# Performance work log

Measured on AMD Instinct MI355X. Metric: run time of the kernel, lower is better.

Reference implementation:

```python
import jax, jax.numpy as jnp
import numpy as np

B, P, K = 32, 2048, 20   # events, points per event, kNN neighbors
EPS = 1e-5               # BatchNorm eps (eval mode, running stats)


def setup_inputs() -> dict:
    key = jax.random.key(0)
    ks = iter(jax.random.split(key, 64))
    inp = {}
    inp["x"] = jax.random.normal(next(ks), (B * P, 7), jnp.float32)
    inp["batch"] = jnp.repeat(jnp.arange(B, dtype=jnp.int32), P)

    def add_layer(tag, cin, cout):
        inp["w" + tag] = jax.random.normal(next(ks), (cin, cout), jnp.float32) / np.sqrt(cin)
        inp["b" + tag] = jax.random.normal(next(ks), (cout,), jnp.float32) * 0.01
        inp["g" + tag] = jax.random.uniform(next(ks), (cout,), jnp.float32, 0.5, 1.5)
        inp["e" + tag] = jax.random.normal(next(ks), (cout,), jnp.float32) * 0.1
        inp["m" + tag] = jax.random.normal(next(ks), (cout,), jnp.float32) * 0.1
        inp["v" + tag] = jax.random.uniform(next(ks), (cout,), jnp.float32, 0.5, 1.5)

    # conv1 MLP: [14, 64, 64, 64]
    add_layer("10", 14, 64)
    add_layer("11", 64, 64)
    add_layer("12", 64, 64)
    # conv2 MLP: [128, 128]
    add_layer("20", 128, 128)
    return inp


def _lin_relu_bn(h, W, b, g, be, rm, rv):
    # Linear -> ReLU -> BatchNorm1d (eval mode: running stats)
    h = jax.nn.relu(h @ W + b)
    return (h - rm) * (g / jnp.sqrt(rv + EPS)) + be


def _knn_idx(x):
    # x: [B, P, C] -> indices of K nearest neighbors (incl. self), [B, P, K]
    sq = jnp.sum(x * x, axis=-1)                                   # [B, P]
    d = sq[:, :, None] + sq[:, None, :] - 2.0 * jnp.einsum("bpc,bqc->bpq", x, x)
    _, idx = jax.lax.top_k(-d, K)
    return idx


def _edge_conv(x, mlp):
    # DynamicEdgeConv: kNN graph on current features, edge MLP([x_i, x_j - x_i]), max-aggr
    idx = _knn_idx(x)                                              # [B, P, K]
    xj = jax.vmap(lambda xb, ib: xb[ib])(x, idx)                   # [B, P, K, C]
    xi = jnp.broadcast_to(x[:, :, None, :], xj.shape)
    e = jnp.concatenate([xi, xj - xi], axis=-1)                    # [B, P, K, 2C]
    return jnp.max(mlp(e), axis=2)                                 # [B, P, Cout]


def reference(x, batch,
              w10, b10, g10, e10, m10, v10,
              w11, b11, g11, e11, m11, v11,
              w12, b12, g12, e12, m12, v12,
              w20, b20, g20, e20, m20, v20):
    xb = x.reshape(B, P, -1)                                       # fixed-size events

    def mlp1(e):
        h = _lin_relu_bn(e, w10, b10, g10, e10, m10, v10)
        h = _lin_relu_bn(h, w11, b11, g11, e11, m11, v11)
        return _lin_relu_bn(h, w12, b12, g12, e12, m12, v12)

    def mlp2(e):
        return _lin_relu_bn(e, w20, b20, g20, e20, m20, v20)

    x1 = _edge_conv(xb, mlp1)                                      # [B, P, 64]
    x2 = _edge_conv(x1, mlp2)                                      # [B, P, 128]
    out = jnp.concatenate([x1, x2], axis=-1).reshape(B * P, 192)
    return out, batch
```

## Files before the change

kernel.cpp:

```cpp
#include <hip/hip_runtime.h>

#define B_EV 32
#define P_PT 2048
#define K_NN 20
#define NPTS (B_EV*P_PT)
#define EPS_BN 1e-5f
#define RINF 3.0e38f

typedef _Float16 half8 __attribute__((ext_vector_type(8)));
typedef float f32x4 __attribute__((ext_vector_type(4)));

static constexpr int oWA10=0, oWB10=448, oB10=896, oT10=960,
  oT11=5184,
  oT12=9408,
  oWA20=9472, oWB20=17664, oB20=25856, oT20=25984,
  oB11p=26048, oB12p=26112,
  oW11hi=26176, oW11lo=28224,
  oW12hi=30272, oW12lo=32320;
static constexpr size_t oIDX = 36864;
static constexpr size_t oA1  = 1347584;
static constexpr size_t oB1  = oA1 + (size_t)NPTS*64;
static constexpr size_t oV2  = oB1 + (size_t)NPTS*64;
static constexpr size_t oX1  = oV2 + (size_t)NPTS*128;
static constexpr size_t oSQ  = oX1 + (size_t)NPTS*64;
static constexpr size_t oX1H = oSQ + (size_t)NPTS;
static constexpr size_t oX1L = oX1H + (size_t)NPTS*32;
static constexpr size_t oU2  = oA1;

__global__ __launch_bounds__(128) void k_prep(
  const float* w10,const float* b10,const float* g10,const float* e10,const float* m10,const float* v10,
  const float* w11,const float* b11,const float* g11,const float* e11,const float* m11,const float* v11,
  const float* w12,const float* b12,const float* g12,const float* e12,const float* m12,const float* v12,
  const float* w20,const float* b20,const float* g20,const float* e20,const float* m20,const float* v20,
  float* ws)
{
  __shared__ float t10s[64], t11s[64];
  int c = threadIdx.x;
  if (c < 64) {
    float s0 = g10[c]*rsqrtf(v10[c]+EPS_BN);
    ws[oB10+c]=b10[c]*s0;
    float t10 = e10[c]-m10[c]*s0; ws[oT10+c]=t10; t10s[c]=t10;
    for (int i=0;i<7;i++){
      ws[oWA10+i*64+c]=(w10[i*64+c]-w10[(7+i)*64+c])*s0;
      ws[oWB10+i*64+c]=w10[(7+i)*64+c]*s0;
    }
    float s1 = g11[c]*rsqrtf(v11[c]+EPS_BN);
    float t11 = e11[c]-m11[c]*s1; ws[oT11+c]=t11; t11s[c]=t11;
    float s2 = g12[c]*rsqrtf(v12[c]+EPS_BN);
    ws[oT12+c]=e12[c]-m12[c]*s2;
  }
  __syncthreads();
  if (c < 64) {
    float s1 = g11[c]*rsqrtf(v11[c]+EPS_BN);
    _Float16* W1hi = (_Float16*)(ws + oW11hi);
    _Float16* W1lo = (_Float16*)(ws + oW11lo);
    float acc = b11[c]*s1;
    for (int i=0;i<64;i++){
      float wv = w11[i*64+c]*s1;
      _Float16 h = (_Float16)wv;
      W1hi[c*64+i] = h;
      W1lo[c*64+i] = (_Float16)(wv - (float)h);
      acc = fmaf(t10s[i], wv, acc);
    }
    ws[oB11p+c]=acc;
    float s2 = g12[c]*rsqrtf(v12[c]+EPS_BN);
    _Float16* W2hi = (_Float16*)(ws + oW12hi);
    _Float16* W2lo = (_Float16*)(ws + oW12lo);
    float acc2 = b12[c]*s2;
    for (int i=0;i<64;i++){
      float wv = w12[i*64+c]*s2;
      _Float16 h = (_Float16)wv;
      W2hi[c*64+i] = h;
      W2lo[c*64+i] = (_Float16)(wv - (float)h);
      acc2 = fmaf(t11s[i], wv, acc2);
    }
    ws[oB12p+c]=acc2;
  }
  {
    float s = g20[c]*rsqrtf(v20[c]+EPS_BN);
    ws[oB20+c]=b20[c]*s; ws[oT20+c]=e20[c]-m20[c]*s;
    for (int i=0;i<64;i++){
      ws[oWA20+i*128+c]=(w20[i*128+c]-w20[(64+i)*128+c])*s;
      ws[oWB20+i*128+c]=w20[(64+i)*128+c]*s;
    }
  }
}

__device__ __forceinline__ void select20(float (&d)[32], int lane, int base, int g,
                                         int* __restrict__ idxout)
{
  float g4[4];
  #pragma unroll
  for (int k=0;k<4;k++){
    float m = d[8*k];
    #pragma unroll
    for (int j=1;j<8;j++) m = fminf(m, d[8*k+j]);
    g4[k]=m;
  }
  float T = 0.f;
  #pragma unroll 1
  for (int pass=0; pass<20; ++pass){
    float m = fminf(fminf(g4[0],g4[1]), fminf(g4[2],g4[3]));
    #pragma unroll
    for (int off=32; off>0; off>>=1) m = fminf(m, __shfl_xor(m, off, 64));
    if (pass==19){ T=m; break; }
    #pragma unroll
    for (int k=0;k<4;k++){
      if (g4[k]==m){
        #pragma unroll
        for (int j=0;j<8;j++) d[8*k+j] = (d[8*k+j]==m) ? RINF : d[8*k+j];
        float mm = d[8*k];
        #pragma unroll
        for (int j=1;j<8;j++) mm = fminf(mm, d[8*k+j]);
        g4[k]=mm;
      }
    }
  }
  int cnt=0;
  #pragma unroll
  for (int j=0;j<32;j++){
    bool take = (d[j]>=RINF) || (d[j]==T);
    unsigned long long mb = __ballot(take);
    if (take){
      int pos = cnt + (int)__popcll(mb & ((1ull<<lane)-1ull));
      if (pos < K_NN) idxout[(size_t)g*K_NN + pos] = base + j*64 + lane;
    }
    cnt += (int)__popcll(mb);
  }
  if (lane==0){
    for (int r=cnt; r<K_NN; ++r) idxout[(size_t)g*K_NN + r] = g;
  }
}

__global__ __launch_bounds__(1024, 8) void k_knn1(const float* __restrict__ x, int* __restrict__ idxout)
{
  __shared__ float xs[P_PT*8];
  int t = threadIdx.x;
  int b = blockIdx.x;
  int xcd = b & 7, kk = b >> 3;
  int e = xcd + ((kk >> 7) << 3);
  int blk = kk & 127;
  {
    const float* xe = x + (size_t)e*P_PT*7;
    #pragma unroll
    for (int u=0; u<2; u++){
      int p = t + u*1024;
      float v0=xe[p*7+0], v1=xe[p*7+1], v2=xe[p*7+2], v3=xe[p*7+3];
      float v4=xe[p*7+4], v5=xe[p*7+5], v6=xe[p*7+6];
      int s = (p&7)<<2;
      int w0 = (p*8) ^ s;
      int w1 = (p*8+4) ^ s;
      f32x4 lo = {v0,v1,v2,v3};
      f32x4 hi = {v4,v5,v6,0.f};
      *(f32x4*)(xs + w0) = lo;
      *(f32x4*)(xs + w1) = hi;
    }
  }
  __syncthreads();
  int lane = t & 63;
  int g = e*P_PT + blk*16 + (t>>6);
  int pin = g & (P_PT-1);
  float xp[7];
  {
    int s = (pin&7)<<2;
    f32x4 lo = *(const f32x4*)(xs + ((pin*8)^s));
    f32x4 hi = *(const f32x4*)(xs + ((pin*8+4)^s));
    xp[0]=lo[0]; xp[1]=lo[1]; xp[2]=lo[2]; xp[3]=lo[3];
    xp[4]=hi[0]; xp[5]=hi[1]; xp[6]=hi[2];
  }
  int sl = (lane&7)<<2;
  const float* base0 = xs + ((lane*8)^sl);
  const float* base1 = xs + ((lane*8+4)^sl);
  float d[32];
  #pragma unroll
  for (int j=0;j<32;j++){
    f32x4 lo = *(const f32x4*)(base0 + j*512);
    f32x4 hi = *(const f32x4*)(base1 + j*512);
    float s=0.f, df;
    df = xp[0]-lo[0]; s=fmaf(df,df,s);
    df = xp[1]-lo[1]; s=fmaf(df,df,s);
    df = xp[2]-lo[2]; s=fmaf(df,df,s);
    df = xp[3]-lo[3]; s=fmaf(df,df,s);
    df = xp[4]-hi[0]; s=fmaf(df,df,s);
    df = xp[5]-hi[1]; s=fmaf(df,df,s);
    df = xp[6]-hi[2]; s=fmaf(df,df,s);
    d[j]=s;
  }
  select20(d, lane, e*P_PT, g, idxout);
}

__global__ __launch_bounds__(256) void k_ab1(const float* __restrict__ x, const float* __restrict__ W,
                                             float* __restrict__ A1, float* __restrict__ B1)
{
  int g = blockIdx.x*256+threadIdx.x;
  float xi[7];
  #pragma unroll
  for (int i=0;i<7;i++) xi[i]=x[(size_t)g*7+i];
  float a[64], b[64];
  #pragma unroll
  for (int c=0;c<64;c++){ a[c]=W[oB10+c]; b[c]=0.f; }
  #pragma unroll
  for (int i=0;i<7;i++){
    #pragma unroll
    for (int c=0;c<64;c++) a[c]=fmaf(xi[i], W[oWA10+i*64+c], a[c]);
    #pragma unroll
    for (int c=0;c<64;c++) b[c]=fmaf(xi[i], W[oWB10+i*64+c], b[c]);
  }
  #pragma unroll
  for (int c=0;c<64;c+=4){
    float4 oa; oa.x=a[c]; oa.y=a[c+1]; oa.z=a[c+2]; oa.w=a[c+3];
    *(float4*)(A1+(size_t)g*64+c)=oa;
    float4 ob; ob.x=b[c]; ob.y=b[c+1]; ob.z=b[c+2]; ob.w=b[c+3];
    *(float4*)(B1+(size_t)g*64+c)=ob;
  }
}

__global__ __launch_bounds__(256, 2) void k_ec1m(const int* __restrict__ idx, const float* __restrict__ ws,
    const float* __restrict__ A1, const float* __restrict__ B1,
    float* __restrict__ x1, _Float16* __restrict__ x1h, _Float16* __restrict__ x1l,
    float* __restrict__ sqv, float* __restrict__ out)
{
  __shared__ float h2s[4][48*64];
  int t = threadIdx.x, w = t>>6, lane = t&63;
  int b = blockIdx.x;
  int xcd = b & 7, kk = b >> 3;
  int ev = xcd + ((kk >> 8) << 3);
  int iA = ev*P_PT + (kk & 255)*8 + w*2;
  int iB = iA + 1;
  int lg = lane>>4, lr = lane&15;

  int jT0 = idx[(size_t)iA*K_NN + lr];
  int jT1 = idx[(size_t)iB*K_NN + lr];
  int a2 = (lr < 4) ? iA*K_NN + 16 + lr : iB*K_NN + 12 + lr;
  a2 = (lr < 8) ? a2 : 0;
  int jT2 = (lr < 8) ? idx[a2] : iA;

  const float* ApA = A1 + (size_t)iA*64;
  const float* ApB = A1 + (size_t)iB*64;
  float4 avA[2][2], avB[2][2], bv[3][2][2];
  const float* Bp0 = B1 + (size_t)jT0*64;
  const float* Bp1 = B1 + (size_t)jT1*64;
  const float* Bp2 = B1 + (size_t)jT2*64;
  #pragma unroll
  for (int ks=0;ks<2;ks++){
    int c0 = ks*32 + lg*8;
    avA[ks][0] = *(const float4*)(ApA+c0); avA[ks][1] = *(const float4*)(ApA+c0+4);
    avB[ks][0] = *(const float4*)(ApB+c0); avB[ks][1] = *(const float4*)(ApB+c0+4);
    bv[0][ks][0] = *(const float4*)(Bp0+c0); bv[0][ks][1] = *(const float4*)(Bp0+c0+4);
    bv[1][ks][0] = *(const float4*)(Bp1+c0); bv[1][ks][1] = *(const float4*)(Bp1+c0+4);
    bv[2][ks][0] = *(const float4*)(Bp2+c0); bv[2][ks][1] = *(const float4*)(Bp2+c0+4);
  }

  bool useB2 = (lr >= 4) && (lr < 8);
  half8 AH[3][2], AL[3][2];
  #pragma unroll
  for (int tile=0;tile<3;tile++){
    #pragma unroll
    for (int ks=0;ks<2;ks++){
      float4 a0, a1;
      if (tile==0){ a0 = avA[ks][0]; a1 = avA[ks][1]; }
      else if (tile==1){ a0 = avB[ks][0]; a1 = avB[ks][1]; }
      else {
        a0.x = useB2 ? avB[ks][0].x : avA[ks][0].x;  a0.y = useB2 ? avB[ks][0].y : avA[ks][0].y;
        a0.z = useB2 ? avB[ks][0].z : avA[ks][0].z;  a0.w = useB2 ? avB[ks][0].w : avA[ks][0].w;
        a1.x = useB2 ? avB[ks][1].x : avA[ks][1].x;  a1.y = useB2 ? avB[ks][1].y : avA[ks][1].y;
        a1.z = useB2 ? avB[ks][1].z : avA[ks][1].z;  a1.w = useB2 ? avB[ks][1].w : avA[ks][1].w;
      }
      float hv[8];
      hv[0]=fmaxf(a0.x+bv[tile][ks][0].x,0.f); hv[1]=fmaxf(a0.y+bv[tile][ks][0].y,0.f);
      hv[2]=fmaxf(a0.z+bv[tile][ks][0].z,0.f); hv[3]=fmaxf(a0.w+bv[tile][ks][0].w,0.f);
      hv[4]=fmaxf(a1.x+bv[tile][ks][1].x,0.f); hv[5]=fmaxf(a1.y+bv[tile][ks][1].y,0.f);
      hv[6]=fmaxf(a1.z+bv[tile][ks][1].z,0.f); hv[7]=fmaxf(a1.w+bv[tile][ks][1].w,0.f);
      half8 ah, al;
      #pragma unroll
      for (int q=0;q<8;q++){
        _Float16 h = (_Float16)hv[q];
        ah[q]=h; al[q]=(_Float16)(hv[q]-(float)h);
      }
      AH[tile][ks]=ah; AL[tile][ks]=al;
    }
  }

  f32x4 acc[3][4];
  #pragma unroll
  for (int nt=0;nt<4;nt++){
    float bb = ws[oB11p + nt*16 + lr];
    f32x4 v = {bb,bb,bb,bb};
    acc[0][nt]=v; acc[1][nt]=v; acc[2][nt]=v;
  }
  {
    const _Float16* W1hi = (const _Float16*)(ws + oW11hi);
    const _Float16* W1lo = (const _Float16*)(ws + oW11lo);
    #pragma unroll
    for (int nt=0;nt<4;nt++){
      const _Float16* whp = W1hi + (nt*16+lr)*64 + lg*8;
      const _Float16* wlp = W1lo + (nt*16+lr)*64 + lg*8;
      half8 wh0 = *(const half8*)(whp);
      half8 wh1 = *(const half8*)(whp+32);
      half8 wl0 = *(const half8*)(wlp);
      half8 wl1 = *(const half8*)(wlp+32);
      #pragma unroll
      for (int tile=0;tile<3;tile++){
        acc[tile][nt] = __builtin_amdgcn_mfma_f32_16x16x32_f16(AH[tile][0], wh0, acc[tile][nt], 0,0,0);
        acc[tile][nt] = __builtin_amdgcn_mfma_f32_16x16x32_f16(AL[tile][0], wh0, acc[tile][nt], 0,0,0);
        acc[tile][nt] = __builtin_amdgcn_mfma_f32_16x16x32_f16(AH[tile][0], wl0, acc[tile][nt], 0,0,0);
        acc[tile][nt] = __builtin_amdgcn_mfma_f32_16x16x32_f16(AH[tile][1], wh1, acc[tile][nt], 0,0,0);
        acc[tile][nt] = __builtin_amdgcn_mfma_f32_16x16x32_f16(AL[tile][1], wh1, acc[tile][nt], 0,0,0);
        acc[tile][nt] = __builtin_amdgcn_mfma_f32_16x16x32_f16(AH[tile][1], wl1, acc[tile][nt], 0,0,0);
      }
    }
  }

  float* hb = h2s[w];
  #pragma unroll
  for (int tile=0;tile<3;tile++){
    #pragma unroll
    for (int nt=0;nt<4;nt++){
      #pragma unroll
      for (int r=0;r<4;r++){
        int row = tile*16 + lg*4 + r;
        int col = nt*16 + lr;
        int baddr = (row*256 + col*4) ^ ((row&7)<<4);
        *(float*)((char*)hb + baddr) = fmaxf(acc[tile][nt][r], 0.f);
      }
    }
  }

  half8 AH2[3][2], AL2[3][2];
  #pragma unroll
  for (int tile=0;tile<3;tile++){
    #pragma unroll
    for (int ks=0;ks<2;ks++){
      int row = tile*16 + lr;
      int byte0 = (row*256 + (ks*32 + lg*8)*4);
      int s = (row&7)<<4;
      f32x4 v0 = *(const f32x4*)((char*)hb + ((byte0)^s));
      f32x4 v1 = *(const f32x4*)((char*)hb + ((byte0+16)^s));
      half8 ah, al;
      #pragma unroll
      for (int q=0;q<4;q++){
        _Float16 h = (_Float16)v0[q];
        ah[q]=h; al[q]=(_Float16)(v0[q]-(float)h);
      }
      #pragma unroll
      for (int q=0;q<4;q++){
        _Float16 h = (_Float16)v1[q];
        ah[4+q]=h; al[4+q]=(_Float16)(v1[q]-(float)h);
      }
      AH2[tile][ks]=ah; AL2[tile][ks]=al;
    }
  }

  f32x4 acc2[3][4];
  #pragma unroll
  for (int nt=0;nt<4;nt++){
    float bb = ws[oB12p + nt*16 + lr];
    f32x4 v = {bb,bb,bb,bb};
    acc2[0][nt]=v; acc2[1][nt]=v; acc2[2][nt]=v;
  }
  {
    const _Float16* W2hi = (const _Float16*)(ws + oW12hi);
    const _Float16* W2lo = (const _Float16*)(ws + oW12lo);
    #pragma unroll
    for (int nt=0;nt<4;nt++){
      const _Float16* whp = W2hi + (nt*16+lr)*64 + lg*8;
      const _Float16* wlp = W2lo + (nt*16+lr)*64 + lg*8;
      half8 wh0 = *(const half8*)(whp);
      half8 wh1 = *(const half8*)(whp+32);
      half8 wl0 = *(const half8*)(wlp);
      half8 wl1 = *(const half8*)(wlp+32);
      #pragma unroll
      for (int tile=0;tile<3;tile++){
        acc2[tile][nt] = __builtin_amdgcn_mfma_f32_16x16x32_f16(AH2[tile][0], wh0, acc2[tile][nt], 0,0,0);
        acc2[tile][nt] = __builtin_amdgcn_mfma_f32_16x16x32_f16(AL2[tile][0], wh0, acc2[tile][nt], 0,0,0);
        acc2[tile][nt] = __builtin_amdgcn_mfma_f32_16x16x32_f16(AH2[tile][0], wl0, acc2[tile][nt], 0,0,0);
        acc2[tile][nt] = __builtin_amdgcn_mfma_f32_16x16x32_f16(AH2[tile][1], wh1, acc2[tile][nt], 0,0,0);
        acc2[tile][nt] = __builtin_amdgcn_mfma_f32_16x16x32_f16(AL2[tile][1], wh1, acc2[tile][nt], 0,0,0);
        acc2[tile][nt] = __builtin_amdgcn_mfma_f32_16x16x32_f16(AH2[tile][1], wl1, acc2[tile][nt], 0,0,0);
      }
    }
  }

  float finA[4], finB[4];
  float sqA = 0.f, sqB = 0.f;
  #pragma unroll
  for (int nt=0;nt<4;nt++){
    float cvA = -RINF;
    #pragma unroll
    for (int r=0;r<4;r++) cvA = fmaxf(cvA, acc2[0][nt][r]);
    if (lg==0){
      #pragma unroll
      for (int r=0;r<4;r++) cvA = fmaxf(cvA, acc2[2][nt][r]);
    }
    cvA = fmaxf(cvA, __shfl_xor(cvA,16,64));
    cvA = fmaxf(cvA, __shfl_xor(cvA,32,64));
    finA[nt] = fmaxf(cvA, 0.f) + ws[oT12 + nt*16 + lr];
    sqA = fmaf(finA[nt], finA[nt], sqA);

    float cvB = -RINF;
    #pragma unroll
    for (int r=0;r<4;r++) cvB = fmaxf(cvB, acc2[1][nt][r]);
    if (lg==1){
      #pragma unroll
      for (int r=0;r<4;r++) cvB = fmaxf(cvB, acc2[2][nt][r]);
    }
    cvB = fmaxf(cvB, __shfl_xor(cvB,16,64));
    cvB = fmaxf(cvB, __shfl_xor(cvB,32,64));
    finB[nt] = fmaxf(cvB, 0.f) + ws[oT12 + nt*16 + lr];
    sqB = fmaf(finB[nt], finB[nt], sqB);
  }
  if (lane < 16){
    #pragma unroll
    for (int nt=0;nt<4;nt++){
      x1[(size_t)iA*64 + nt*16 + lane] = finA[nt];
      out[(size_t)iA*192 + nt*16 + lane] = finA[nt];
      x1[(size_t)iB*64 + nt*16 + lane] = finB[nt];
      out[(size_t)iB*192 + nt*16 + lane] = finB[nt];
      _Float16 hA = (_Float16)finA[nt];
      x1h[(size_t)iA*64 + nt*16 + lane] = hA;
      x1l[(size_t)iA*64 + nt*16 + lane] = (_Float16)(finA[nt]-(float)hA);
      _Float16 hB = (_Float16)finB[nt];
      x1h[(size_t)iB*64 + nt*16 + lane] = hB;
      x1l[(size_t)iB*64 + nt*16 + lane] = (_Float16)(finB[nt]-(float)hB);
    }
  }
  #pragma unroll
  for (int off=1; off<16; off<<=1){
    sqA += __shfl_xor(sqA, off, 64);
    sqB += __shfl_xor(sqB, off, 64);
  }
  if (lane == 0){ sqv[iA] = sqA; sqv[iB] = sqB; }
}

__global__ __launch_bounds__(1024, 4) void k_dsel(const _Float16* __restrict__ x1h,
    const _Float16* __restrict__ x1l, const float* __restrict__ sqv, int* __restrict__ idxout)
{
  __shared__ float cs[16][520];
  int t = threadIdx.x, w = t>>6, lane = t&63;
  int b = blockIdx.x;
  int xcd = b & 7, kk = b >> 3;
  int e = xcd + ((kk >> 7) << 3);
  int base16 = e*P_PT + (kk & 127)*16;
  int lg = lane>>4, lr = lane&15;

  half8 AH[2], AL[2];
  {
    const _Float16* Ah = x1h + (size_t)(base16 + lr)*64;
    const _Float16* Al = x1l + (size_t)(base16 + lr)*64;
    #pragma unroll
    for (int kx=0;kx<2;kx++){
      AH[kx] = *(const half8*)(Ah + kx*32 + lg*8);
      AL[kx] = *(const half8*)(Al + kx*32 + lg*8);
    }
  }
  int p = base16 + w;
  float sqp = sqv[p];
  const _Float16* Xh = x1h + (size_t)e*P_PT*64;
  const _Float16* Xl = x1l + (size_t)e*P_PT*64;
  const float* sqe = sqv + e*P_PT;

  float d[32];
  #pragma unroll 1
  for (int cc=0; cc<4; ++cc){
    #pragma unroll
    for (int hh=0; hh<2; hh++){
      int c = cc*512 + hh*256 + w*16 + lr;
      const _Float16* Bh = Xh + (size_t)c*64;
      const _Float16* Bl = Xl + (size_t)c*64;
      f32x4 acc = {0.f,0.f,0.f,0.f};
      #pragma unroll
      for (int kx=0;kx<2;kx++){
        half8 bh = *(const half8*)(Bh + kx*32 + lg*8);
        half8 bl = *(const half8*)(Bl + kx*32 + lg*8);
        acc = __builtin_amdgcn_mfma_f32_16x16x32_f16(AH[kx], bh, acc, 0,0,0);
        acc = __builtin_amdgcn_mfma_f32_16x16x32_f16(AL[kx], bh, acc, 0,0,0);
        acc = __builtin_amdgcn_mfma_f32_16x16x32_f16(AH[kx], bl, acc, 0,0,0);
        acc = __builtin_amdgcn_mfma_f32_16x16x32_f16(AL[kx], bl, acc, 0,0,0);
      }
      #pragma unroll
      for (int r=0;r<4;r++) cs[4*lg + r][hh*256 + w*16 + lr] = acc[r];
    }
    __syncthreads();
    #pragma unroll
    for (int jj=0;jj<8;jj++){
      float sqc = sqe[cc*512 + jj*64 + lane];
      d[cc*8 + jj] = sqp + sqc - 2.f*cs[w][jj*64 + lane];
    }
    __syncthreads();
  }
  select20(d, lane, e*P_PT, p, idxout);
}

__global__ __launch_bounds__(256) void k_uv2(const float* __restrict__ x1, const float* __restrict__ W,
                                             float* __restrict__ U2, float* __restrict__ V2)
{
  int g = blockIdx.x*256 + threadIdx.x;
  int half = blockIdx.y & 1;
  bool isU = blockIdx.y < 2;
  const float* Wb = W + (isU?oWA20:oWB20) + half*64;
  float acc[64];
  #pragma unroll
  for (int c=0;c<64;c++) acc[c] = isU ? W[oB20+half*64+c] : 0.f;
  const float* xp = x1 + (size_t)g*64;
  #pragma unroll 1
  for (int i=0;i<64;i+=4){
    float4 xv = *(const float4*)(xp+i);
    #pragma unroll
    for (int c=0;c<64;c++) acc[c]=fmaf(xv.x, Wb[(i+0)*128+c], acc[c]);
    #pragma unroll
    for (int c=0;c<64;c++) acc[c]=fmaf(xv.y, Wb[(i+1)*128+c], acc[c]);
    #pragma unroll
    for (int c=0;c<64;c++) acc[c]=fmaf(xv.z, Wb[(i+2)*128+c], acc[c]);
    #pragma unroll
    for (int c=0;c<64;c++) acc[c]=fmaf(xv.w, Wb[(i+3)*128+c], acc[c]);
  }
  float* dst = (isU?U2:V2) + (size_t)g*128 + half*64;
  #pragma unroll
  for (int c=0;c<64;c+=4){
    float4 o; o.x=acc[c]; o.y=acc[c+1]; o.z=acc[c+2]; o.w=acc[c+3];
    *(float4*)(dst+c)=o;
  }
}

__global__ __launch_bounds__(256) void k_gather2(const int* __restrict__ idx, const float* __restrict__ U2,
     const float* __restrict__ V2, const float* __restrict__ W, const int* __restrict__ batch,
     float* __restrict__ out)
{
  int b = blockIdx.x;
  int xcd = b & 7, kk = b >> 3;
  int ev = xcd + ((kk >> 3) << 3);
  int g = ev*P_PT + (kk & 7)*256 + threadIdx.x;
  int half = blockIdx.y;
  if (half == 0) out[(size_t)NPTS*192 + g] = (float)batch[g];
  float mx[64];
  #pragma unroll
  for (int c=0;c<64;c++) mx[c]=-RINF;
  for (int k=0;k<K_NN;k++){
    int j = idx[(size_t)g*K_NN+k];
    const float4* vp = (const float4*)(V2 + (size_t)j*128 + half*64);
    #pragma unroll
    for (int c4=0;c4<16;c4++){
      float4 v=vp[c4];
      mx[c4*4+0]=fmaxf(mx[c4*4+0],v.x);
      mx[c4*4+1]=fmaxf(mx[c4*4+1],v.y);
      mx[c4*4+2]=fmaxf(mx[c4*4+2],v.z);
      mx[c4*4+3]=fmaxf(mx[c4*4+3],v.w);
    }
  }
  const float* Up = U2 + (size_t)g*128 + half*64;
  float* op = out + (size_t)g*192 + 64 + half*64;
  #pragma unroll
  for (int c=0;c<64;c+=4){
    float4 o;
    o.x = fmaxf(Up[c+0]+mx[c+0],0.f)+W[oT20+half*64+c+0];
    o.y = fmaxf(Up[c+1]+mx[c+1],0.f)+W[oT20+half*64+c+1];
    o.z = fmaxf(Up[c+2]+mx[c+2],0.f)+W[oT20+half*64+c+2];
    o.w = fmaxf(Up[c+3]+mx[c+3],0.f)+W[oT20+half*64+c+3];
    *(float4*)(op+c)=o;
  }
}

extern "C" void kernel_launch(void* const* d_in, const int* in_sizes, int n_in,
                              void* d_out, int out_size, void* d_ws, size_t ws_size,
                              hipStream_t stream)
{
  const float* x     = (const float*)d_in[0];
  const int*   batch = (const int*)d_in[1];
  const float* w10=(const float*)d_in[2],  *b10=(const float*)d_in[3],  *g10=(const float*)d_in[4],
             *e10=(const float*)d_in[5],  *m10=(const float*)d_in[6],  *v10=(const float*)d_in[7];
  const float* w11=(const float*)d_in[8],  *b11=(const float*)d_in[9],  *g11=(const float*)d_in[10],
             *e11=(const float*)d_in[11], *m11=(const float*)d_in[12], *v11=(const float*)d_in[13];
  const float* w12=(const float*)d_in[14], *b12=(const float*)d_in[15], *g12=(const float*)d_in[16],
             *e12=(const float*)d_in[17], *m12=(const float*)d_in[18], *v12=(const float*)d_in[19];
  const float* w20=(const float*)d_in[20], *b20=(const float*)d_in[21], *g20=(const float*)d_in[22],
             *e20=(const float*)d_in[23], *m20=(const float*)d_in[24], *v20=(const float*)d_in[25];

  float* ws  = (float*)d_ws;
  float* out = (float*)d_out;
  int*   idxp = (int*)(ws + oIDX);
  _Float16* x1h = (_Float16*)(ws + oX1H);
  _Float16* x1l = (_Float16*)(ws + oX1L);

  k_prep<<<1,128,0,stream>>>(w10,b10,g10,e10,m10,v10, w11,b11,g11,e11,m11,v11,
                             w12,b12,g12,e12,m12,v12, w20,b20,g20,e20,m20,v20, ws);
  k_knn1<<<NPTS/16, 1024, 0, stream>>>(x, idxp);
  k_ab1<<<NPTS/256, 256, 0, stream>>>(x, ws, ws+oA1, ws+oB1);
  k_ec1m<<<NPTS/8, 256, 0, stream>>>(idxp, ws, ws+oA1, ws+oB1, ws+oX1, x1h, x1l, ws+oSQ, out);
  k_dsel<<<NPTS/16, 1024, 0, stream>>>(x1h, x1l, ws+oSQ, idxp);
  k_uv2<<<dim3(NPTS/256,4),256,0,stream>>>(ws+oX1, ws, ws+oU2, ws+oV2);
  k_gather2<<<dim3(NPTS/256,2),256,0,stream>>>(idxp, ws+oU2, ws+oV2, ws, batch, out);
}
```

Measured before the change: 1.057 ms.

## Double-buffer kNN distance tile in LDS and interleave independent MFMA chains

```diff
diff --git a/kernel.cpp b/kernel.cpp
--- a/kernel.cpp
+++ b/kernel.cpp
@@ -435,7 +435,7 @@
 __global__ __launch_bounds__(1024, 4) void k_dsel(const _Float16* __restrict__ x1h,
     const _Float16* __restrict__ x1l, const float* __restrict__ sqv, int* __restrict__ idxout)
 {
-  __shared__ float cs[16][520];
+  __shared__ float cs[2][16][512];
   int t = threadIdx.x, w = t>>6, lane = t&63;
   int b = blockIdx.x;
   int xcd = b & 7, kk = b >> 3;
@@ -458,35 +458,53 @@
   const _Float16* Xh = x1h + (size_t)e*P_PT*64;
   const _Float16* Xl = x1l + (size_t)e*P_PT*64;
   const float* sqe = sqv + e*P_PT;
+  int rsw = (w&7)<<2;
 
   float d[32];
-  #pragma unroll 1
+  #pragma unroll
   for (int cc=0; cc<4; ++cc){
-    #pragma unroll
-    for (int hh=0; hh<2; hh++){
-      int c = cc*512 + hh*256 + w*16 + lr;
-      const _Float16* Bh = Xh + (size_t)c*64;
-      const _Float16* Bl = Xl + (size_t)c*64;
-      f32x4 acc = {0.f,0.f,0.f,0.f};
-      #pragma unroll
-      for (int kx=0;kx<2;kx++){
-        half8 bh = *(const half8*)(Bh + kx*32 + lg*8);
-        half8 bl = *(const half8*)(Bl + kx*32 + lg*8);
-        acc = __builtin_amdgcn_mfma_f32_16x16x32_f16(AH[kx], bh, acc, 0,0,0);
-        acc = __builtin_amdgcn_mfma_f32_16x16x32_f16(AL[kx], bh, acc, 0,0,0);
-        acc = __builtin_amdgcn_mfma_f32_16x16x32_f16(AH[kx], bl, acc, 0,0,0);
-        acc = __builtin_amdgcn_mfma_f32_16x16x32_f16(AL[kx], bl, acc, 0,0,0);
-      }
-      #pragma unroll
-      for (int r=0;r<4;r++) cs[4*lg + r][hh*256 + w*16 + lr] = acc[r];
-    }
+    int buf = cc & 1;
+    int c0 = cc*512 +       w*16 + lr;
+    int c1 = cc*512 + 256 + w*16 + lr;
+    const _Float16* B0h = Xh + (size_t)c0*64;
+    const _Float16* B0l = Xl + (size_t)c0*64;
+    const _Float16* B1h = Xh + (size_t)c1*64;
+    const _Float16* B1l = Xl + (size_t)c1*64;
+    half8 b0h[2], b0l[2], b1h[2], b1l[2];
+    #pragma unroll
+    for (int kx=0;kx<2;kx++){
+      b0h[kx] = *(const half8*)(B0h + kx*32 + lg*8);
+      b0l[kx] = *(const half8*)(B0l + kx*32 + lg*8);
+      b1h[kx] = *(const half8*)(B1h + kx*32 + lg*8);
+      b1l[kx] = *(const half8*)(B1l + kx*32 + lg*8);
+    }
+    f32x4 a0 = {0.f,0.f,0.f,0.f}, a1 = {0.f,0.f,0.f,0.f};
+    #pragma unroll
+    for (int kx=0;kx<2;kx++){
+      a0 = __builtin_amdgcn_mfma_f32_16x16x32_f16(AH[kx], b0h[kx], a0, 0,0,0);
+      a1 = __builtin_amdgcn_mfma_f32_16x16x32_f16(AH[kx], b1h[kx], a1, 0,0,0);
+      a0 = __builtin_amdgcn_mfma_f32_16x16x32_f16(AL[kx], b0h[kx], a0, 0,0,0);
+      a1 = __builtin_amdgcn_mfma_f32_16x16x32_f16(AL[kx], b1h[kx], a1, 0,0,0);
+      a0 = __builtin_amdgcn_mfma_f32_16x16x32_f16(AH[kx], b0l[kx], a0, 0,0,0);
+      a1 = __builtin_amdgcn_mfma_f32_16x16x32_f16(AH[kx], b1l[kx], a1, 0,0,0);
+      a0 = __builtin_amdgcn_mfma_f32_16x16x32_f16(AL[kx], b0l[kx], a0, 0,0,0);
+      a1 = __builtin_amdgcn_mfma_f32_16x16x32_f16(AL[kx], b1l[kx], a1, 0,0,0);
+    }
+    #pragma unroll
+    for (int r=0;r<4;r++){
+      int row = 4*lg + r;
+      int sw = (row&7)<<2;
+      cs[buf][row][(      w*16 + lr) ^ sw] = a0[r];
+      cs[buf][row][(256 + w*16 + lr) ^ sw] = a1[r];
+    }
+    float sqr[8];
+    #pragma unroll
+    for (int jj=0;jj<8;jj++) sqr[jj] = sqe[cc*512 + jj*64 + lane];
     __syncthreads();
     #pragma unroll
     for (int jj=0;jj<8;jj++){
-      float sqc = sqe[cc*512 + jj*64 + lane];
-      d[cc*8 + jj] = sqp + sqc - 2.f*cs[w][jj*64 + lane];
-    }
-    __syncthreads();
+      d[cc*8 + jj] = sqp + sqr[jj] - 2.f*cs[buf][w][(jj*64 + lane) ^ rsw];
+    }
   }
   select20(d, lane, e*P_PT, p, idxout);
 }
```

After: 1.018 ms. 1.04x faster.

## Double-buffer distance tile in LDS with XOR swizzle, drop second barrier

Applied to the files above, without the earlier changes.

```diff
diff --git a/kernel.cpp b/kernel.cpp
--- a/kernel.cpp
+++ b/kernel.cpp
@@ -435,7 +435,7 @@
 __global__ __launch_bounds__(1024, 4) void k_dsel(const _Float16* __restrict__ x1h,
     const _Float16* __restrict__ x1l, const float* __restrict__ sqv, int* __restrict__ idxout)
 {
-  __shared__ float cs[16][520];
+  __shared__ float cs[2][16][512];
   int t = threadIdx.x, w = t>>6, lane = t&63;
   int b = blockIdx.x;
   int xcd = b & 7, kk = b >> 3;
@@ -443,25 +443,19 @@
   int base16 = e*P_PT + (kk & 127)*16;
   int lg = lane>>4, lr = lane&15;
 
-  half8 AH[2], AL[2];
-  {
-    const _Float16* Ah = x1h + (size_t)(base16 + lr)*64;
-    const _Float16* Al = x1l + (size_t)(base16 + lr)*64;
-    #pragma unroll
-    for (int kx=0;kx<2;kx++){
-      AH[kx] = *(const half8*)(Ah + kx*32 + lg*8);
-      AL[kx] = *(const half8*)(Al + kx*32 + lg*8);
-    }
-  }
+  const _Float16* Ah = x1h + (size_t)(base16 + lr)*64 + lg*8;
+  const _Float16* Al = x1l + (size_t)(base16 + lr)*64 + lg*8;
   int p = base16 + w;
   float sqp = sqv[p];
-  const _Float16* Xh = x1h + (size_t)e*P_PT*64;
-  const _Float16* Xl = x1l + (size_t)e*P_PT*64;
+  const _Float16* Xh = x1h + (size_t)e*P_PT*64 + lg*8;
+  const _Float16* Xl = x1l + (size_t)e*P_PT*64 + lg*8;
   const float* sqe = sqv + e*P_PT;
+  int rsw = (w&7)<<2;
 
   float d[32];
-  #pragma unroll 1
+  #pragma unroll
   for (int cc=0; cc<4; ++cc){
+    int buf = cc & 1;
     #pragma unroll
     for (int hh=0; hh<2; hh++){
       int c = cc*512 + hh*256 + w*16 + lr;
@@ -470,23 +464,29 @@
       f32x4 acc = {0.f,0.f,0.f,0.f};
       #pragma unroll
       for (int kx=0;kx<2;kx++){
-        half8 bh = *(const half8*)(Bh + kx*32 + lg*8);
-        half8 bl = *(const half8*)(Bl + kx*32 + lg*8);
-        acc = __builtin_amdgcn_mfma_f32_16x16x32_f16(AH[kx], bh, acc, 0,0,0);
-        acc = __builtin_amdgcn_mfma_f32_16x16x32_f16(AL[kx], bh, acc, 0,0,0);
-        acc = __builtin_amdgcn_mfma_f32_16x16x32_f16(AH[kx], bl, acc, 0,0,0);
-        acc = __builtin_amdgcn_mfma_f32_16x16x32_f16(AL[kx], bl, acc, 0,0,0);
-      }
-      #pragma unroll
-      for (int r=0;r<4;r++) cs[4*lg + r][hh*256 + w*16 + lr] = acc[r];
-    }
+        half8 ah = *(const half8*)(Ah + kx*32);
+        half8 al = *(const half8*)(Al + kx*32);
+        half8 bh = *(const half8*)(Bh + kx*32);
+        half8 bl = *(const half8*)(Bl + kx*32);
+        acc = __builtin_amdgcn_mfma_f32_16x16x32_f16(ah, bh, acc, 0,0,0);
+        acc = __builtin_amdgcn_mfma_f32_16x16x32_f16(al, bh, acc, 0,0,0);
+        acc = __builtin_amdgcn_mfma_f32_16x16x32_f16(ah, bl, acc, 0,0,0);
+        acc = __builtin_amdgcn_mfma_f32_16x16x32_f16(al, bl, acc, 0,0,0);
+      }
+      #pragma unroll
+      for (int r=0;r<4;r++){
+        int row = 4*lg + r;
+        cs[buf][row][(hh*256 + w*16 + lr) ^ ((row&7)<<2)] = acc[r];
+      }
+    }
+    float sqr[8];
+    #pragma unroll
+    for (int jj=0;jj<8;jj++) sqr[jj] = sqe[cc*512 + jj*64 + lane];
     __syncthreads();
     #pragma unroll
     for (int jj=0;jj<8;jj++){
-      float sqc = sqe[cc*512 + jj*64 + lane];
-      d[cc*8 + jj] = sqp + sqc - 2.f*cs[w][jj*64 + lane];
-    }
-    __syncthreads();
+      d[cc*8 + jj] = sqp + sqr[jj] - 2.f*cs[buf][w][(jj*64 + lane) ^ rsw];
+    }
   }
   select20(d, lane, e*P_PT, p, idxout);
 }
```

After: 1.101 ms. 1.04x slower.

## Shrink distance-select blocks to 8 query points with single-pass LDS tile

Applied to the files above, without the earlier changes.

```diff
diff --git a/kernel.cpp b/kernel.cpp
--- a/kernel.cpp
+++ b/kernel.cpp
@@ -432,61 +432,55 @@
   if (lane == 0){ sqv[iA] = sqA; sqv[iB] = sqB; }
 }
 
-__global__ __launch_bounds__(1024, 4) void k_dsel(const _Float16* __restrict__ x1h,
+__global__ __launch_bounds__(512, 4) void k_dsel8(const _Float16* __restrict__ x1h,
     const _Float16* __restrict__ x1l, const float* __restrict__ sqv, int* __restrict__ idxout)
 {
-  __shared__ float cs[16][520];
+  __shared__ float cs[8][2048];
   int t = threadIdx.x, w = t>>6, lane = t&63;
   int b = blockIdx.x;
   int xcd = b & 7, kk = b >> 3;
-  int e = xcd + ((kk >> 7) << 3);
-  int base16 = e*P_PT + (kk & 127)*16;
+  int e = xcd + ((kk >> 8) << 3);
+  int base8 = e*P_PT + (kk & 255)*8;
   int lg = lane>>4, lr = lane&15;
 
-  half8 AH[2], AL[2];
   {
-    const _Float16* Ah = x1h + (size_t)(base16 + lr)*64;
-    const _Float16* Al = x1l + (size_t)(base16 + lr)*64;
-    #pragma unroll
-    for (int kx=0;kx<2;kx++){
-      AH[kx] = *(const half8*)(Ah + kx*32 + lg*8);
-      AL[kx] = *(const half8*)(Al + kx*32 + lg*8);
-    }
-  }
-  int p = base16 + w;
-  float sqp = sqv[p];
-  const _Float16* Xh = x1h + (size_t)e*P_PT*64;
-  const _Float16* Xl = x1l + (size_t)e*P_PT*64;
-  const float* sqe = sqv + e*P_PT;
-
-  float d[32];
-  #pragma unroll 1
-  for (int cc=0; cc<4; ++cc){
-    #pragma unroll
-    for (int hh=0; hh<2; hh++){
-      int c = cc*512 + hh*256 + w*16 + lr;
+    half8 AH[2], AL[2];
+    const _Float16* Ah = x1h + (size_t)(base8 + (lr&7))*64 + lg*8;
+    const _Float16* Al = x1l + (size_t)(base8 + (lr&7))*64 + lg*8;
+    AH[0] = *(const half8*)(Ah);     AH[1] = *(const half8*)(Ah + 32);
+    AL[0] = *(const half8*)(Al);     AL[1] = *(const half8*)(Al + 32);
+    const _Float16* Xh = x1h + (size_t)e*P_PT*64 + lg*8;
+    const _Float16* Xl = x1l + (size_t)e*P_PT*64 + lg*8;
+    #pragma unroll 4
+    for (int tt=0; tt<16; ++tt){
+      int c = w*256 + tt*16 + lr;
       const _Float16* Bh = Xh + (size_t)c*64;
       const _Float16* Bl = Xl + (size_t)c*64;
       f32x4 acc = {0.f,0.f,0.f,0.f};
       #pragma unroll
       for (int kx=0;kx<2;kx++){
-        half8 bh = *(const half8*)(Bh + kx*32 + lg*8);
-        half8 bl = *(const half8*)(Bl + kx*32 + lg*8);
+        half8 bh = *(const half8*)(Bh + kx*32);
+        half8 bl = *(const half8*)(Bl + kx*32);
         acc = __builtin_amdgcn_mfma_f32_16x16x32_f16(AH[kx], bh, acc, 0,0,0);
         acc = __builtin_amdgcn_mfma_f32_16x16x32_f16(AL[kx], bh, acc, 0,0,0);
         acc = __builtin_amdgcn_mfma_f32_16x16x32_f16(AH[kx], bl, acc, 0,0,0);
         acc = __builtin_amdgcn_mfma_f32_16x16x32_f16(AL[kx], bl, acc, 0,0,0);
       }
-      #pragma unroll
-      for (int r=0;r<4;r++) cs[4*lg + r][hh*256 + w*16 + lr] = acc[r];
-    }
-    __syncthreads();
-    #pragma unroll
-    for (int jj=0;jj<8;jj++){
-      float sqc = sqe[cc*512 + jj*64 + lane];
-      d[cc*8 + jj] = sqp + sqc - 2.f*cs[w][jj*64 + lane];
-    }
-    __syncthreads();
+      if (lg < 2){
+        #pragma unroll
+        for (int r=0;r<4;r++) cs[4*lg + r][w*256 + tt*16 + lr] = acc[r];
+      }
+    }
+  }
+  __syncthreads();
+
+  int p = base8 + w;
+  float sqp = sqv[p];
+  const float* sqe = sqv + e*P_PT;
+  float d[32];
+  #pragma unroll
+  for (int j=0;j<32;j++){
+    d[j] = sqp + sqe[j*64 + lane] - 2.f*cs[w][j*64 + lane];
   }
   select20(d, lane, e*P_PT, p, idxout);
 }
@@ -586,7 +580,7 @@
   k_knn1<<<NPTS/16, 1024, 0, stream>>>(x, idxp);
   k_ab1<<<NPTS/256, 256, 0, stream>>>(x, ws, ws+oA1, ws+oB1);
   k_ec1m<<<NPTS/8, 256, 0, stream>>>(idxp, ws, ws+oA1, ws+oB1, ws+oX1, x1h, x1l, ws+oSQ, out);
-  k_dsel<<<NPTS/16, 1024, 0, stream>>>(x1h, x1l, ws+oSQ, idxp);
+  k_dsel8<<<NPTS/8, 512, 0, stream>>>(x1h, x1l, ws+oSQ, idxp);
   k_uv2<<<dim3(NPTS/256,4),256,0,stream>>>(ws+oX1, ws, ws+oU2, ws+oV2);
   k_gather2<<<dim3(NPTS/256,2),256,0,stream>>>(idxp, ws+oU2, ws+oV2, ws, batch, out);
 }
```

Measured after the change: 1.119 ms. +5.8%, slower.
